# Optimization experiments

Measured on AMD Instinct MI355X. Metric: run time of the kernel, lower is better.

## Reference

```python
import jax, jax.numpy as jnp
import numpy as np

DIM = 300

def setup_inputs() -> dict:
    key = jax.random.key(0)
    k1, k2 = jax.random.split(key)
    article_concat = jax.random.normal(k1, (256, 2048, DIM), dtype=jnp.float32)
    options_concat = jax.random.normal(k2, (256, 64, DIM), dtype=jnp.float32)
    return {"article_concat": article_concat, "options_concat": options_concat}

def reference(article_concat, options_concat):
    # Mean-pool over the word dimension for both inputs, then concat features.
    article_mean = jnp.mean(article_concat, axis=1)   # [B, DIM]
    options_mean = jnp.mean(options_concat, axis=1)   # [B, DIM]
    return jnp.concatenate([article_mean, options_mean], axis=1)  # [B, 2*DIM]
```

## Files before the change

### kernel.cpp

```cpp
#include <hip/hip_runtime.h>


#define B        256
#define DIM      300
#define J4       75
#define W_ART    2048
#define W_OPT    64
#define ART_SPLIT 8
#define ROWS_ART (W_ART / ART_SPLIT)

__global__ __launch_bounds__(DIM) void meanpool_concat_kernel(
    const float4* __restrict__ art,
    const float4* __restrict__ opt,
    float* __restrict__ out)
{
    const int b    = blockIdx.x;
    const int y    = blockIdx.y;
    const int t    = threadIdx.x;
    const int rsub = t / J4;
    const int j    = t % J4;

    __shared__ float4 lds[DIM];

    float4 acc = make_float4(0.f, 0.f, 0.f, 0.f);

    if (y < ART_SPLIT) {
        const float4* slab = art + (size_t)b * (W_ART * J4);
        const int w0 = y * ROWS_ART;
        #pragma unroll 4
        for (int it = 0; it < ROWS_ART / 4; ++it) {
            const int w = w0 + it * 4 + rsub;
            const float4 v = slab[(size_t)w * J4 + j];
            acc.x += v.x; acc.y += v.y; acc.z += v.z; acc.w += v.w;
        }
        lds[t] = acc;
        __syncthreads();
        if (t < J4) {
            const float4 a = lds[t], bb = lds[t + J4],
                         c = lds[t + 2 * J4], d = lds[t + 3 * J4];
            const float s = 1.0f / (float)W_ART;
            float* o = out + (size_t)b * (2 * DIM) + 4 * t;
            atomicAdd(o + 0, (a.x + bb.x + c.x + d.x) * s);
            atomicAdd(o + 1, (a.y + bb.y + c.y + d.y) * s);
            atomicAdd(o + 2, (a.z + bb.z + c.z + d.z) * s);
            atomicAdd(o + 3, (a.w + bb.w + c.w + d.w) * s);
        }
    } else {
        const float4* slab = opt + (size_t)b * (W_OPT * J4);
        #pragma unroll 4
        for (int it = 0; it < W_OPT / 4; ++it) {
            const int w = it * 4 + rsub;
            const float4 v = slab[(size_t)w * J4 + j];
            acc.x += v.x; acc.y += v.y; acc.z += v.z; acc.w += v.w;
        }
        lds[t] = acc;
        __syncthreads();
        if (t < J4) {
            const float4 a = lds[t], bb = lds[t + J4],
                         c = lds[t + 2 * J4], d = lds[t + 3 * J4];
            const float s = 1.0f / (float)W_OPT;
            float* o = out + (size_t)b * (2 * DIM) + DIM + 4 * t;
            o[0] = (a.x + bb.x + c.x + d.x) * s;
            o[1] = (a.y + bb.y + c.y + d.y) * s;
            o[2] = (a.z + bb.z + c.z + d.z) * s;
            o[3] = (a.w + bb.w + c.w + d.w) * s;
        }
    }
}

extern "C" void kernel_launch(void* const* d_in, const int* in_sizes, int n_in,
                              void* d_out, int out_size, void* d_ws, size_t ws_size,
                              hipStream_t stream) {
    const float4* art = (const float4*)d_in[0];
    const float4* opt = (const float4*)d_in[1];
    float* out = (float*)d_out;

    hipMemsetAsync(d_out, 0, (size_t)out_size * sizeof(float), stream);

    dim3 grid(B, ART_SPLIT + 1);
    dim3 block(DIM);
    meanpool_concat_kernel<<<grid, block, 0, stream>>>(art, opt, out);
}
```

Baseline: 806.2 us.

## Replace atomic accumulation with partial-sum workspace and finalize kernel

Splits the work into two kernels: the first writes each article slab's partial sums to a workspace instead of atomically adding into the output. A second kernel sums those partials and also computes the options mean, which removes the memset and the atomics. The article loop now reads a contiguous slab with linear indexing and two accumulators to raise memory-level parallelism. The cost is an extra kernel launch and a small workspace round trip.

```diff
diff --git a/kernel.cpp b/kernel.cpp
--- a/kernel.cpp
+++ b/kernel.cpp
@@ -6,78 +6,81 @@
 #define J4       75
 #define W_ART    2048
 #define W_OPT    64
-#define ART_SPLIT 8
-#define ROWS_ART (W_ART / ART_SPLIT)
+#define SPLIT    8
+#define ROWS_PB  (W_ART / SPLIT)
+#define ITERS    (ROWS_PB * J4 / DIM)
 
-__global__ __launch_bounds__(DIM) void meanpool_concat_kernel(
+__global__ __launch_bounds__(DIM) void art_partial_kernel(
     const float4* __restrict__ art,
-    const float4* __restrict__ opt,
+    float4* __restrict__ part)
+{
+    const int b = blockIdx.x;
+    const int y = blockIdx.y;
+    const int t = threadIdx.x;
+    const int j = t % J4;
+
+    const float4* base = art + (size_t)b * (W_ART * J4) + (size_t)y * (ROWS_PB * J4);
+
+    float4 a0 = make_float4(0.f, 0.f, 0.f, 0.f);
+    float4 a1 = make_float4(0.f, 0.f, 0.f, 0.f);
+    #pragma unroll 4
+    for (int it = 0; it < ITERS; it += 2) {
+        const float4 v0 = base[(size_t)(it + 0) * DIM + t];
+        const float4 v1 = base[(size_t)(it + 1) * DIM + t];
+        a0.x += v0.x; a0.y += v0.y; a0.z += v0.z; a0.w += v0.w;
+        a1.x += v1.x; a1.y += v1.y; a1.z += v1.z; a1.w += v1.w;
+    }
+    a0.x += a1.x; a0.y += a1.y; a0.z += a1.z; a0.w += a1.w;
+
+    __shared__ float4 lds[DIM];
+    lds[t] = a0;
+    __syncthreads();
+    if (t < J4) {
+        const float4 p0 = lds[t],          p1 = lds[t + J4],
+                     p2 = lds[t + 2 * J4], p3 = lds[t + 3 * J4];
+        float4 r;
+        r.x = p0.x + p1.x + p2.x + p3.x;
+        r.y = p0.y + p1.y + p2.y + p3.y;
+        r.z = p0.z + p1.z + p2.z + p3.z;
+        r.w = p0.w + p1.w + p2.w + p3.w;
+        part[((size_t)y * B + b) * J4 + j] = r;
+    }
+}
+
+__global__ __launch_bounds__(DIM) void finalize_kernel(
+    const float* __restrict__ part,
+    const float* __restrict__ opt,
     float* __restrict__ out)
 {
-    const int b    = blockIdx.x;
-    const int y    = blockIdx.y;
-    const int t    = threadIdx.x;
-    const int rsub = t / J4;
-    const int j    = t % J4;
+    const int b = blockIdx.x;
+    const int c = threadIdx.x;
 
-    __shared__ float4 lds[DIM];
+    float s = 0.f;
+    #pragma unroll
+    for (int y = 0; y < SPLIT; ++y)
+        s += part[((size_t)y * B + b) * DIM + c];
 
-    float4 acc = make_float4(0.f, 0.f, 0.f, 0.f);
+    const float* ob = opt + (size_t)b * (W_OPT * DIM);
+    float o0 = 0.f, o1 = 0.f;
+    #pragma unroll 4
+    for (int w = 0; w < W_OPT; w += 2) {
+        o0 += ob[(size_t)(w + 0) * DIM + c];
+        o1 += ob[(size_t)(w + 1) * DIM + c];
+    }
 
-    if (y < ART_SPLIT) {
-        const float4* slab = art + (size_t)b * (W_ART * J4);
-        const int w0 = y * ROWS_ART;
-        #pragma unroll 4
-        for (int it = 0; it < ROWS_ART / 4; ++it) {
-            const int w = w0 + it * 4 + rsub;
-            const float4 v = slab[(size_t)w * J4 + j];
-            acc.x += v.x; acc.y += v.y; acc.z += v.z; acc.w += v.w;
-        }
-        lds[t] = acc;
-        __syncthreads();
-        if (t < J4) {
-            const float4 a = lds[t], bb = lds[t + J4],
-                         c = lds[t + 2 * J4], d = lds[t + 3 * J4];
-            const float s = 1.0f / (float)W_ART;
-            float* o = out + (size_t)b * (2 * DIM) + 4 * t;
-            atomicAdd(o + 0, (a.x + bb.x + c.x + d.x) * s);
-            atomicAdd(o + 1, (a.y + bb.y + c.y + d.y) * s);
-            atomicAdd(o + 2, (a.z + bb.z + c.z + d.z) * s);
-            atomicAdd(o + 3, (a.w + bb.w + c.w + d.w) * s);
-        }
-    } else {
-        const float4* slab = opt + (size_t)b * (W_OPT * J4);
-        #pragma unroll 4
-        for (int it = 0; it < W_OPT / 4; ++it) {
-            const int w = it * 4 + rsub;
-            const float4 v = slab[(size_t)w * J4 + j];
-            acc.x += v.x; acc.y += v.y; acc.z += v.z; acc.w += v.w;
-        }
-        lds[t] = acc;
-        __syncthreads();
-        if (t < J4) {
-            const float4 a = lds[t], bb = lds[t + J4],
-                         c = lds[t + 2 * J4], d = lds[t + 3 * J4];
-            const float s = 1.0f / (float)W_OPT;
-            float* o = out + (size_t)b * (2 * DIM) + DIM + 4 * t;
-            o[0] = (a.x + bb.x + c.x + d.x) * s;
-            o[1] = (a.y + bb.y + c.y + d.y) * s;
-            o[2] = (a.z + bb.z + c.z + d.z) * s;
-            o[3] = (a.w + bb.w + c.w + d.w) * s;
-        }
-    }
+    float* ou = out + (size_t)b * (2 * DIM);
+    ou[c]       = s * (1.0f / (float)W_ART);
+    ou[DIM + c] = (o0 + o1) * (1.0f / (float)W_OPT);
 }
 
 extern "C" void kernel_launch(void* const* d_in, const int* in_sizes, int n_in,
                               void* d_out, int out_size, void* d_ws, size_t ws_size,
                               hipStream_t stream) {
     const float4* art = (const float4*)d_in[0];
-    const float4* opt = (const float4*)d_in[1];
-    float* out = (float*)d_out;
+    const float*  opt = (const float*)d_in[1];
+    float* out  = (float*)d_out;
+    float4* part = (float4*)d_ws;
 
-    hipMemsetAsync(d_out, 0, (size_t)out_size * sizeof(float), stream);
-
-    dim3 grid(B, ART_SPLIT + 1);
-    dim3 block(DIM);
-    meanpool_concat_kernel<<<grid, block, 0, stream>>>(art, opt, out);
+    art_partial_kernel<<<dim3(B, SPLIT), dim3(DIM), 0, stream>>>(art, part);
+    finalize_kernel<<<dim3(B), dim3(DIM), 0, stream>>>((const float*)part, opt, out);
 }
```

Measured after the change: 804.1 us. No clear change (-0.3%).
